# Performance work log

Measured on AMD Instinct MI355X. Metric: run time of the kernel, lower is better.

The kernel has to match this reference:

```python
import jax, jax.numpy as jnp
import numpy as np

B, L = 4, 2048
D_Q = D_K = D_V = 512
D_MODEL = 512
H = 8  # heads; head dim = D_MODEL // H = 64


def _conv1x1(x, W, b):
    # Conv1d with kernel_size=1 == pointwise linear over channels.
    # x: (B, C_in, L), W: (C_out, C_in), b: (C_out,) -> (B, C_out, L)
    return jnp.einsum('oc,bcl->bol', W, x) + b[None, :, None]


def setup_inputs() -> dict:
    key = jax.random.key(0)
    ks = jax.random.split(key, 12)
    s = 0.02
    return {
        'q': jax.random.normal(ks[0], (B, D_Q, L), jnp.float32),
        'k': jax.random.normal(ks[1], (B, D_K, L), jnp.float32),
        'v': jax.random.normal(ks[2], (B, D_V, L), jnp.float32),
        'input_mask': jnp.ones((B, 1, L), jnp.float32),
        'Wq': jax.random.normal(ks[3], (D_MODEL, D_Q), jnp.float32) * s,
        'bq': jax.random.normal(ks[4], (D_MODEL,), jnp.float32) * s,
        'Wk': jax.random.normal(ks[5], (D_MODEL, D_K), jnp.float32) * s,
        'bk': jax.random.normal(ks[6], (D_MODEL,), jnp.float32) * s,
        'Wv': jax.random.normal(ks[7], (D_MODEL, D_V), jnp.float32) * s,
        'bv': jax.random.normal(ks[8], (D_MODEL,), jnp.float32) * s,
        'Wout': jax.random.normal(ks[9], (D_V, D_MODEL), jnp.float32) * s,
        'bout': jax.random.normal(ks[10], (D_V,), jnp.float32) * s,
    }


def reference(q, k, v, input_mask, Wq, bq, Wk, bk, Wv, bv, Wout, bout):
    Bq, _, Lq = q.shape
    qh = _conv1x1(q, Wq, bq).reshape(Bq, H, -1, Lq)  # (B,H,D,L)
    kh = _conv1x1(k, Wk, bk).reshape(Bq, H, -1, Lq)
    vh = _conv1x1(v, Wv, bv).reshape(Bq, H, -1, Lq)
    Dh = qh.shape[2]
    scale = 1.0 / jnp.sqrt(jnp.asarray(Dh, qh.dtype))
    scores = jnp.einsum('bhdl,bhdn->bhln', qh, kh) * scale  # (B,H,L,L)
    # total_mask = ~input_mask[:, 0:1, :].bool(); True -> masked keys
    pad = input_mask[:, 0:1, :] <= 0.5  # (B,1,L_k)
    scores = jnp.where(pad[:, None, :, :], jnp.asarray(-1e9, scores.dtype), scores)
    attn = jax.nn.softmax(scores, axis=-1)  # attn_dropout is None in module
    out = jnp.einsum('bhdn,bhln->bhdl', vh, attn).reshape(Bq, -1, Lq)  # (B,d_model,L)
    # self.dropout is identity at inference; final 1x1 conv projection
    return _conv1x1(out, Wout, bout)  # (B, d_v, L)
```

## Files before the change

kernel.cpp:

```cpp
#include <hip/hip_runtime.h>
#include <hip/hip_bf16.h>


#define BB  4
#define LL  2048
#define CC  512
#define HH  8
#define DHH 64

typedef __attribute__((ext_vector_type(8)))  short bf16x8;
typedef __attribute__((ext_vector_type(4)))  short bf16x4;
typedef __attribute__((ext_vector_type(16))) float f32x16;
typedef __attribute__((ext_vector_type(2)))  unsigned uint2v;
typedef __attribute__((ext_vector_type(4)))  unsigned uint4v;

using us = unsigned short;

#if __has_builtin(__builtin_amdgcn_exp2f)
#define EXP2(x) __builtin_amdgcn_exp2f(x)
#else
#define EXP2(x) __expf(0.6931471805599453f * (x))
#endif

__device__ __forceinline__ int swz(int r) { return (r + (r >> 3)) & 7; }

__device__ __forceinline__ us f2bu(float x) {
    unsigned u = __float_as_uint(x);
    return (us)((u + 0x7FFFu + ((u >> 16) & 1u)) >> 16);
}
__device__ __forceinline__ unsigned pk2(float a, float b) {
    unsigned r;
    asm("v_cvt_pk_bf16_f32 %0, %1, %2" : "=v"(r) : "v"(a), "v"(b));
    return r;
}
__device__ __forceinline__ bf16x4 pk4(float a, float b, float c, float d) {
    uint2v u; u[0] = pk2(a, b); u[1] = pk2(c, d);
    return __builtin_bit_cast(bf16x4, u);
}

__device__ __forceinline__ void transpose_body(const float* __restrict__ X,
                                               us* __restrict__ Xt,
                                               int b, int c0, int n0, int t)
{
    __shared__ float T[64][65];

    const float* Xb = X + ((size_t)b * CC + c0) * LL + n0;
    #pragma unroll
    for (int i = 0; i < 4; ++i) {
        const int cl = (t >> 4) + 16 * i, nl = (t & 15) * 4;
        const float4 f = *(const float4*)(Xb + (size_t)cl * LL + nl);
        T[cl][nl + 0] = f.x; T[cl][nl + 1] = f.y;
        T[cl][nl + 2] = f.z; T[cl][nl + 3] = f.w;
    }
    __syncthreads();
    us* Ot = Xt + ((size_t)b * LL + n0) * CC + c0;
    #pragma unroll
    for (int i = 0; i < 2; ++i) {
        const int nl = (t >> 3) + 32 * i, cb = (t & 7) * 8;
        uint4v u;
        #pragma unroll
        for (int j = 0; j < 4; ++j)
            u[j] = pk2(T[cb + 2 * j][nl], T[cb + 2 * j + 1][nl]);
        *(bf16x8*)(Ot + (size_t)nl * CC + cb) = __builtin_bit_cast(bf16x8, u);
    }
}

__global__ __launch_bounds__(256) void transpose_cvt(const float* __restrict__ X,
                                                     us* __restrict__ Xt)
{
    transpose_body(X, Xt, blockIdx.z, blockIdx.y * 64, blockIdx.x * 64, threadIdx.x);
}

__global__ __launch_bounds__(256) void transpose_cvt3(
    const float* __restrict__ Xq, const float* __restrict__ Xk,
    const float* __restrict__ Xv,
    us* __restrict__ X0, us* __restrict__ X1, us* __restrict__ X2)
{
    const int z = blockIdx.z, which = z >> 2, b = z & 3;
    const float* X = which == 0 ? Xq : (which == 1 ? Xk : Xv);
    us* Xt = which == 0 ? X0 : (which == 1 ? X1 : X2);
    transpose_body(X, Xt, b, blockIdx.y * 64, blockIdx.x * 64, threadIdx.x);
}

__global__ __launch_bounds__(256) void cvt_w4(const float* __restrict__ W0,
                                              const float* __restrict__ W1,
                                              const float* __restrict__ W2,
                                              const float* __restrict__ W3,
                                              us* __restrict__ out)
{
    const float* Ws[4] = {W0, W1, W2, W3};
    const float* W = Ws[blockIdx.y];
    us* O = out + (size_t)blockIdx.y * (CC * CC);
    const int i = (blockIdx.x * 256 + threadIdx.x) * 8;
    const float4 f0 = *(const float4*)(W + i);
    const float4 f1 = *(const float4*)(W + i + 4);
    uint4v u;
    u[0] = pk2(f0.x, f0.y); u[1] = pk2(f0.z, f0.w);
    u[2] = pk2(f1.x, f1.y); u[3] = pk2(f1.z, f1.w);
    *(bf16x8*)(O + i) = __builtin_bit_cast(bf16x8, u);
}

__device__ __forceinline__ void proj_body(const us* __restrict__ Xb,
                                          const us* __restrict__ Wm,
                                          const float* __restrict__ bias,
                                          float scale, void* __restrict__ Yv,
                                          int b, int n0, int m0, int t, int mode)
{
    const int lane = t & 63, wave = t >> 6;
    const int quad2 = lane >> 5, l31 = lane & 31;
    const int wr = (wave >> 1) * 64, wc = (wave & 1) * 64;

    __shared__ us As[2][128 * 64];
    __shared__ us Bs[2][128 * 64];
    __shared__ float biasS[128];

    f32x16 acc[2][2];
    #pragma unroll
    for (int mi = 0; mi < 2; ++mi)
        #pragma unroll
        for (int ni = 0; ni < 2; ++ni)
            #pragma unroll
            for (int e = 0; e < 16; ++e) acc[mi][ni][e] = 0.f;

    if (t < 128) biasS[t] = bias[m0 + t];

    #pragma unroll
    for (int i = 0; i < 4; ++i) {
        const int id = i * 256 + t, r = id >> 3, bk = id & 7;
        *(bf16x8*)(As[0] + r * 64 + ((bk ^ swz(r)) * 8)) =
            *(const bf16x8*)(Wm + (size_t)r * CC + bk * 8);
        *(bf16x8*)(Bs[0] + r * 64 + ((bk ^ swz(r)) * 8)) =
            *(const bf16x8*)(Xb + (size_t)(n0 + r) * CC + bk * 8);
    }
    __syncthreads();

    for (int it = 0; it < CC / 64; ++it) {
        const int cur = it & 1, k1 = (it + 1) * 64;

        bf16x8 apre[4], bpre[4];
        if (it + 1 < CC / 64) {
            #pragma unroll
            for (int i = 0; i < 4; ++i) {
                const int id = i * 256 + t, r = id >> 3, bk = id & 7;
                apre[i] = *(const bf16x8*)(Wm + (size_t)r * CC + k1 + bk * 8);
                bpre[i] = *(const bf16x8*)(Xb + (size_t)(n0 + r) * CC + k1 + bk * 8);
            }
        }

        __builtin_amdgcn_s_setprio(1);
        #pragma unroll
        for (int ks = 0; ks < 4; ++ks) {
            const int bk = quad2 + 2 * ks;
            const int ra0 = wr + l31, ra1 = ra0 + 32;
            const int rb0 = wc + l31, rb1 = rb0 + 32;
            const bf16x8 af0 = *(const bf16x8*)(As[cur] + ra0 * 64 + ((bk ^ swz(ra0)) * 8));
            const bf16x8 af1 = *(const bf16x8*)(As[cur] + ra1 * 64 + ((bk ^ swz(ra1)) * 8));
            const bf16x8 bf0 = *(const bf16x8*)(Bs[cur] + rb0 * 64 + ((bk ^ swz(rb0)) * 8));
            const bf16x8 bf1 = *(const bf16x8*)(Bs[cur] + rb1 * 64 + ((bk ^ swz(rb1)) * 8));
            acc[0][0] = __builtin_amdgcn_mfma_f32_32x32x16_bf16(af0, bf0, acc[0][0], 0, 0, 0);
            acc[0][1] = __builtin_amdgcn_mfma_f32_32x32x16_bf16(af0, bf1, acc[0][1], 0, 0, 0);
            acc[1][0] = __builtin_amdgcn_mfma_f32_32x32x16_bf16(af1, bf0, acc[1][0], 0, 0, 0);
            acc[1][1] = __builtin_amdgcn_mfma_f32_32x32x16_bf16(af1, bf1, acc[1][1], 0, 0, 0);
        }
        __builtin_amdgcn_s_setprio(0);

        if (it + 1 < CC / 64) {
            #pragma unroll
            for (int i = 0; i < 4; ++i) {
                const int id = i * 256 + t, r = id >> 3, bk = id & 7;
                *(bf16x8*)(As[1 - cur] + r * 64 + ((bk ^ swz(r)) * 8)) = apre[i];
                *(bf16x8*)(Bs[1 - cur] + r * 64 + ((bk ^ swz(r)) * 8)) = bpre[i];
            }
        }
        __syncthreads();
    }

    #pragma unroll
    for (int mi = 0; mi < 2; ++mi)
        #pragma unroll
        for (int ni = 0; ni < 2; ++ni) {
            const int nloc = wc + ni * 32 + l31;
            if (mode == 0) {
                us* Y = (us*)Yv;
                #pragma unroll
                for (int rg2 = 0; rg2 < 4; ++rg2) {
                    const int rbase = wr + mi * 32 + 8 * rg2 + 4 * quad2;
                    float v0 = (acc[mi][ni][rg2 * 4 + 0] + biasS[rbase + 0]) * scale;
                    float v1 = (acc[mi][ni][rg2 * 4 + 1] + biasS[rbase + 1]) * scale;
                    float v2 = (acc[mi][ni][rg2 * 4 + 2] + biasS[rbase + 2]) * scale;
                    float v3 = (acc[mi][ni][rg2 * 4 + 3] + biasS[rbase + 3]) * scale;
                    const int mg = m0 + rbase;
                    const int h = mg >> 6, d = mg & 63;
                    *(bf16x4*)(Y + (((size_t)(b * HH + h) * LL) + n0 + nloc) * DHH + d) =
                        pk4(v0, v1, v2, v3);
                }
            } else {
                #pragma unroll
                for (int reg = 0; reg < 16; ++reg) {
                    const int row = (reg & 3) + 8 * (reg >> 2) + 4 * quad2;
                    const int mloc = wr + mi * 32 + row;
                    const float v = (acc[mi][ni][reg] + biasS[mloc]) * scale;
                    const size_t addr = ((size_t)b * CC + m0 + mloc) * LL + n0 + nloc;
                    if (mode == 1) ((us*)Yv)[addr] = f2bu(v);
                    else           ((float*)Yv)[addr] = v;
                }
            }
        }
}

template <int MODE>
__global__ __launch_bounds__(256, 2) void proj_gemm(const us* __restrict__ Xt,
                                                    const us* __restrict__ Wb,
                                                    const float* __restrict__ bias,
                                                    float scale,
                                                    void* __restrict__ Yv)
{
    const int b = blockIdx.z, n0 = blockIdx.x * 128, m0 = blockIdx.y * 128;
    proj_body(Xt + (size_t)b * LL * CC, Wb + (size_t)m0 * CC, bias, scale, Yv,
              b, n0, m0, threadIdx.x, MODE);
}

__global__ __launch_bounds__(256, 2) void proj_gemm3(
    const us* __restrict__ X0, const us* __restrict__ X1, const us* __restrict__ X2,
    const us* __restrict__ Wb4,
    const float* __restrict__ bq, const float* __restrict__ bk,
    const float* __restrict__ bv, float scale_q,
    us* __restrict__ qh, us* __restrict__ kh, us* __restrict__ vh)
{
    const int z = blockIdx.z, which = z >> 2, b = z & 3;
    const int n0 = blockIdx.x * 128, m0 = blockIdx.y * 128;
    const us* Xt = which == 0 ? X0 : (which == 1 ? X1 : X2);
    const us* Wb = Wb4 + (size_t)which * (CC * CC);
    const float* bias = which == 0 ? bq : (which == 1 ? bk : bv);
    const float scale = which == 0 ? scale_q : 1.0f;
    us* Yv = which == 0 ? qh : (which == 1 ? kh : vh);
    const int mode = (which == 2) ? 1 : 0;
    proj_body(Xt + (size_t)b * LL * CC, Wb + (size_t)m0 * CC, bias, scale,
              (void*)Yv, b, n0, m0, threadIdx.x, mode);
}

__global__ __launch_bounds__(256, 2) void attn_fwd(
    const us* __restrict__ Qh,
    const us* __restrict__ Kh,
    const us* __restrict__ Vh,
    const float* __restrict__ mask,
    us* __restrict__ ctx)
{
    const int bh = blockIdx.x;
    const int b = bh >> 3, h = bh & 7;
    const int qb = blockIdx.y;
    const int t = threadIdx.x, lane = t & 63, wave = t >> 6;
    const int quad2 = lane >> 5, l31 = lane & 31;
    const int qg = qb * 128 + wave * 32;
    const int NT = LL / 64;

    __shared__ us Ks[2][64 * 64];
    __shared__ us Vs[2][64 * 64];
    __shared__ unsigned long long mwS[32];

    const float* mb = mask + (size_t)b * LL;
    #pragma unroll
    for (int i = 0; i < 8; ++i) {
        const int tile = wave * 8 + i;
        const unsigned long long bal = __ballot(mb[tile * 64 + lane] > 0.5f);
        if (lane == 0) mwS[tile] = bal;
    }

    const us* Qbase = Qh + (size_t)bh * LL * DHH;
    bf16x8 qf[4];
    #pragma unroll
    for (int ks = 0; ks < 4; ++ks)
        qf[ks] = *(const bf16x8*)(Qbase + (size_t)(qg + l31) * DHH + ks * 16 + quad2 * 8);

    f32x16 of[2];
    #pragma unroll
    for (int mt = 0; mt < 2; ++mt)
        #pragma unroll
        for (int e = 0; e < 16; ++e) of[mt][e] = 0.f;
    float l_run = 0.f;

    const us* Kbase = Kh + (size_t)bh * LL * DHH;
    const us* Vbase = Vh + ((size_t)b * CC + h * DHH) * LL;

    #pragma unroll
    for (int i = 0; i < 2; ++i) {
        const int id = i * 256 + t;
        const int r = id >> 3, bk = id & 7;
        *(bf16x8*)(Ks[0] + r * 64 + ((bk ^ swz(r)) * 8)) =
            *(const bf16x8*)(Kbase + (size_t)r * DHH + bk * 8);
        *(bf16x8*)(Vs[0] + r * 64 + ((bk ^ swz(r)) * 8)) =
            *(const bf16x8*)(Vbase + (size_t)r * LL + bk * 8);
    }
    __syncthreads();

    f32x16 sf[2];
    #pragma unroll
    for (int mt = 0; mt < 2; ++mt)
        #pragma unroll
        for (int e = 0; e < 16; ++e) sf[mt][e] = 0.f;
    __builtin_amdgcn_s_setprio(1);
    #pragma unroll
    for (int ks = 0; ks < 4; ++ks) {
        const int bk = quad2 + 2 * ks;
        #pragma unroll
        for (int mt = 0; mt < 2; ++mt) {
            const int r = mt * 32 + l31;
            const bf16x8 af = *(const bf16x8*)(Ks[0] + r * 64 + ((bk ^ swz(r)) * 8));
            sf[mt] = __builtin_amdgcn_mfma_f32_32x32x16_bf16(af, qf[ks], sf[mt], 0, 0, 0);
        }
    }
    __builtin_amdgcn_s_setprio(0);

    for (int it = 0; it < NT; ++it) {
        const int cur = it & 1;

        bf16x8 kpre[2], vpre[2];
        if (it + 1 < NT) {
            const int n1 = (it + 1) * 64;
            #pragma unroll
            for (int i = 0; i < 2; ++i) {
                const int id = i * 256 + t;
                const int r = id >> 3, bk = id & 7;
                kpre[i] = *(const bf16x8*)(Kbase + (size_t)(n1 + r) * DHH + bk * 8);
                vpre[i] = *(const bf16x8*)(Vbase + (size_t)r * LL + n1 + bk * 8);
            }
        }

        const unsigned long long mw = mwS[it];
        const bool masked = (mw != 0xFFFFFFFFFFFFFFFFull);
        float ps = 0.f;
        bf16x8 pfrag[4];
        #pragma unroll
        for (int mt = 0; mt < 2; ++mt) {
            float p[16];
            #pragma unroll
            for (int e = 0; e < 16; ++e) p[e] = EXP2(sf[mt][e]);
            if (masked) {
                #pragma unroll
                for (int e = 0; e < 16; ++e) {
                    const int row = 32 * mt + (e & 3) + 8 * (e >> 2) + 4 * quad2;
                    p[e] = ((mw >> row) & 1ull) ? p[e] : 0.f;
                }
            }
            const float s0 = (p[0] + p[1]) + (p[2] + p[3]);
            const float s1 = (p[4] + p[5]) + (p[6] + p[7]);
            const float s2 = (p[8] + p[9]) + (p[10] + p[11]);
            const float s3 = (p[12] + p[13]) + (p[14] + p[15]);
            ps += (s0 + s1) + (s2 + s3);
            #pragma unroll
            for (int g = 0; g < 2; ++g) {
                unsigned w0 = pk2(p[8 * g + 0], p[8 * g + 1]);
                unsigned w1 = pk2(p[8 * g + 2], p[8 * g + 3]);
                unsigned w2 = pk2(p[8 * g + 4], p[8 * g + 5]);
                unsigned w3 = pk2(p[8 * g + 6], p[8 * g + 7]);
                asm("v_permlane32_swap_b32 %0, %1" : "+v"(w0), "+v"(w2));
                asm("v_permlane32_swap_b32 %0, %1" : "+v"(w1), "+v"(w3));
                uint4v u; u[0] = w0; u[1] = w1; u[2] = w2; u[3] = w3;
                pfrag[2 * mt + g] = __builtin_bit_cast(bf16x8, u);
            }
        }
        ps += __shfl_xor(ps, 32, 64);
        l_run += ps;

        __builtin_amdgcn_s_setprio(1);
        #pragma unroll
        for (int ks = 0; ks < 4; ++ks) {
            const int bk = quad2 + 2 * ks;
            #pragma unroll
            for (int mt = 0; mt < 2; ++mt) {
                const int r = mt * 32 + l31;
                const bf16x8 vf = *(const bf16x8*)(Vs[cur] + r * 64 + ((bk ^ swz(r)) * 8));
                of[mt] = __builtin_amdgcn_mfma_f32_32x32x16_bf16(vf, pfrag[ks], of[mt], 0, 0, 0);
            }
        }
        __builtin_amdgcn_s_setprio(0);

        if (it + 1 < NT) {
            #pragma unroll
            for (int i = 0; i < 2; ++i) {
                const int id = i * 256 + t;
                const int r = id >> 3, bk = id & 7;
                *(bf16x8*)(Ks[1 - cur] + r * 64 + ((bk ^ swz(r)) * 8)) = kpre[i];
                *(bf16x8*)(Vs[1 - cur] + r * 64 + ((bk ^ swz(r)) * 8)) = vpre[i];
            }
        }
        __syncthreads();

        if (it + 1 < NT) {
            #pragma unroll
            for (int mt = 0; mt < 2; ++mt)
                #pragma unroll
                for (int e = 0; e < 16; ++e) sf[mt][e] = 0.f;
            __builtin_amdgcn_s_setprio(1);
            #pragma unroll
            for (int ks = 0; ks < 4; ++ks) {
                const int bk = quad2 + 2 * ks;
                #pragma unroll
                for (int mt = 0; mt < 2; ++mt) {
                    const int r = mt * 32 + l31;
                    const bf16x8 af = *(const bf16x8*)(Ks[1 - cur] + r * 64 + ((bk ^ swz(r)) * 8));
                    sf[mt] = __builtin_amdgcn_mfma_f32_32x32x16_bf16(af, qf[ks], sf[mt], 0, 0, 0);
                }
            }
            __builtin_amdgcn_s_setprio(0);
        }
    }

    us* Cb = ctx + (size_t)b * LL * CC;
    const float inv = 1.0f / l_run;
    const int q = qg + l31;
    #pragma unroll
    for (int mt = 0; mt < 2; ++mt)
        #pragma unroll
        for (int rg2 = 0; rg2 < 4; ++rg2) {
            const int d = 32 * mt + 8 * rg2 + 4 * quad2;
            *(bf16x4*)(Cb + (size_t)q * CC + h * DHH + d) =
                pk4(of[mt][rg2 * 4 + 0] * inv, of[mt][rg2 * 4 + 1] * inv,
                    of[mt][rg2 * 4 + 2] * inv, of[mt][rg2 * 4 + 3] * inv);
        }
}

extern "C" void kernel_launch(void* const* d_in, const int* in_sizes, int n_in,
                              void* d_out, int out_size, void* d_ws, size_t ws_size,
                              hipStream_t stream)
{
    const float* q    = (const float*)d_in[0];
    const float* k    = (const float*)d_in[1];
    const float* v    = (const float*)d_in[2];
    const float* mask = (const float*)d_in[3];
    const float* Wq   = (const float*)d_in[4];
    const float* bq   = (const float*)d_in[5];
    const float* Wk   = (const float*)d_in[6];
    const float* bk   = (const float*)d_in[7];
    const float* Wv   = (const float*)d_in[8];
    const float* bv   = (const float*)d_in[9];
    const float* Wout = (const float*)d_in[10];
    const float* bout = (const float*)d_in[11];

    const size_t TSZ  = (size_t)BB * CC * LL;
    const size_t WSZ  = (size_t)4 * CC * CC;
    const float SCALE_Q = 0.125f * 1.4426950408889634f;

    const dim3 tb(256), gb(256);

    if (ws_size >= (6 * TSZ + WSZ) * sizeof(us)) {
        us* X0  = (us*)d_ws;
        us* X1  = X0 + TSZ;
        us* X2  = X1 + TSZ;
        us* qh  = X2 + TSZ;
        us* kh  = qh + TSZ;
        us* vh  = kh + TSZ;
        us* Wb  = vh + TSZ;
        us* ctx = X0;

        cvt_w4<<<dim3(CC * CC / 2048, 4), tb, 0, stream>>>(Wq, Wk, Wv, Wout, Wb);
        transpose_cvt3<<<dim3(LL / 64, CC / 64, 12), tb, 0, stream>>>(q, k, v, X0, X1, X2);
        proj_gemm3<<<dim3(LL / 128, CC / 128, 12), gb, 0, stream>>>(
            X0, X1, X2, Wb, bq, bk, bv, SCALE_Q, qh, kh, vh);
        attn_fwd<<<dim3(HH * BB, LL / 128), tb, 0, stream>>>(qh, kh, vh, mask, ctx);
        proj_gemm<2><<<dim3(LL / 128, CC / 128, BB), gb, 0, stream>>>(
            ctx, Wb + 3 * (size_t)CC * CC, bout, 1.0f, d_out);
    } else {
        us* Xt  = (us*)d_ws;
        us* qh  = Xt + TSZ;
        us* kh  = qh + TSZ;
        us* vh  = kh + TSZ;
        us* Wb  = vh + TSZ;
        us* ctx = Xt;

        const dim3 tg(LL / 64, CC / 64, BB), gg(LL / 128, CC / 128, BB);

        cvt_w4<<<dim3(CC * CC / 2048, 4), tb, 0, stream>>>(Wq, Wk, Wv, Wout, Wb);
        transpose_cvt<<<tg, tb, 0, stream>>>(q, Xt);
        proj_gemm<0><<<gg, gb, 0, stream>>>(Xt, Wb + 0 * (size_t)CC * CC, bq, SCALE_Q, (void*)qh);
        transpose_cvt<<<tg, tb, 0, stream>>>(k, Xt);
        proj_gemm<0><<<gg, gb, 0, stream>>>(Xt, Wb + 1 * (size_t)CC * CC, bk, 1.0f, (void*)kh);
        transpose_cvt<<<tg, tb, 0, stream>>>(v, Xt);
        proj_gemm<1><<<gg, gb, 0, stream>>>(Xt, Wb + 2 * (size_t)CC * CC, bv, 1.0f, (void*)vh);
        attn_fwd<<<dim3(HH * BB, LL / 128), tb, 0, stream>>>(qh, kh, vh, mask, ctx);
        proj_gemm<2><<<gg, gb, 0, stream>>>(ctx, Wb + 3 * (size_t)CC * CC, bout, 1.0f, d_out);
    }
}
```

Measured before the change: 192.6 us.

## Split KV loop across two wave groups and use padded k-major LDS layouts

The attention kernel now launches 512 threads per block. Two groups of four waves each process half of the key/value tiles for the same 128 queries, and the partial outputs and row sums are combined through shared memory at the end. This doubles the waves per CU and halves the serial key loop, since the grid is only about one block per CU. Both the projection GEMM and the attention kernel also replace the XOR-swizzled LDS tiles with a padded k-chunk-major layout that uses precomputed byte offsets, cutting address arithmetic and bank conflicts. The combine step only adds the partial sums, so it is correct only if both halves use the same softmax max reference; it also needs more LDS per block.

```diff
diff --git a/kernel.cpp b/kernel.cpp
--- a/kernel.cpp
+++ b/kernel.cpp
@@ -21,8 +21,6 @@
 #else
 #define EXP2(x) __expf(0.6931471805599453f * (x))
 #endif
-
-__device__ __forceinline__ int swz(int r) { return (r + (r >> 3)) & 7; }
 
 __device__ __forceinline__ us f2bu(float x) {
     unsigned u = __float_as_uint(x);
@@ -110,8 +108,7 @@
     const int quad2 = lane >> 5, l31 = lane & 31;
     const int wr = (wave >> 1) * 64, wc = (wave & 1) * 64;
 
-    __shared__ us As[2][128 * 64];
-    __shared__ us Bs[2][128 * 64];
+    __shared__ __align__(16) char PS[66048];
     __shared__ float biasS[128];
 
     f32x16 acc[2][2];
@@ -124,24 +121,30 @@
 
     if (t < 128) biasS[t] = bias[m0 + t];
 
+    const int wrO = (t & 7) * 2064 + (t >> 3) * 16;
+    const int rdA = quad2 * 2064 + (wr + l31) * 16;
+    const int rdB = 16512 + quad2 * 2064 + (wc + l31) * 16;
+
     #pragma unroll
     for (int i = 0; i < 4; ++i) {
-        const int id = i * 256 + t, r = id >> 3, bk = id & 7;
-        *(bf16x8*)(As[0] + r * 64 + ((bk ^ swz(r)) * 8)) =
+        const int r = i * 32 + (t >> 3), bk = t & 7;
+        *(bf16x8*)(PS + wrO + i * 512) =
             *(const bf16x8*)(Wm + (size_t)r * CC + bk * 8);
-        *(bf16x8*)(Bs[0] + r * 64 + ((bk ^ swz(r)) * 8)) =
+        *(bf16x8*)(PS + 16512 + wrO + i * 512) =
             *(const bf16x8*)(Xb + (size_t)(n0 + r) * CC + bk * 8);
     }
     __syncthreads();
 
     for (int it = 0; it < CC / 64; ++it) {
         const int cur = it & 1, k1 = (it + 1) * 64;
+        char* PB = PS + (cur ? 33024 : 0);
+        char* PN = PS + (cur ? 0 : 33024);
 
         bf16x8 apre[4], bpre[4];
         if (it + 1 < CC / 64) {
             #pragma unroll
             for (int i = 0; i < 4; ++i) {
-                const int id = i * 256 + t, r = id >> 3, bk = id & 7;
+                const int r = i * 32 + (t >> 3), bk = t & 7;
                 apre[i] = *(const bf16x8*)(Wm + (size_t)r * CC + k1 + bk * 8);
                 bpre[i] = *(const bf16x8*)(Xb + (size_t)(n0 + r) * CC + k1 + bk * 8);
             }
@@ -150,13 +153,10 @@
         __builtin_amdgcn_s_setprio(1);
         #pragma unroll
         for (int ks = 0; ks < 4; ++ks) {
-            const int bk = quad2 + 2 * ks;
-            const int ra0 = wr + l31, ra1 = ra0 + 32;
-            const int rb0 = wc + l31, rb1 = rb0 + 32;
-            const bf16x8 af0 = *(const bf16x8*)(As[cur] + ra0 * 64 + ((bk ^ swz(ra0)) * 8));
-            const bf16x8 af1 = *(const bf16x8*)(As[cur] + ra1 * 64 + ((bk ^ swz(ra1)) * 8));
-            const bf16x8 bf0 = *(const bf16x8*)(Bs[cur] + rb0 * 64 + ((bk ^ swz(rb0)) * 8));
-            const bf16x8 bf1 = *(const bf16x8*)(Bs[cur] + rb1 * 64 + ((bk ^ swz(rb1)) * 8));
+            const bf16x8 af0 = *(const bf16x8*)(PB + rdA + ks * 4128);
+            const bf16x8 af1 = *(const bf16x8*)(PB + rdA + ks * 4128 + 512);
+            const bf16x8 bf0 = *(const bf16x8*)(PB + rdB + ks * 4128);
+            const bf16x8 bf1 = *(const bf16x8*)(PB + rdB + ks * 4128 + 512);
             acc[0][0] = __builtin_amdgcn_mfma_f32_32x32x16_bf16(af0, bf0, acc[0][0], 0, 0, 0);
             acc[0][1] = __builtin_amdgcn_mfma_f32_32x32x16_bf16(af0, bf1, acc[0][1], 0, 0, 0);
             acc[1][0] = __builtin_amdgcn_mfma_f32_32x32x16_bf16(af1, bf0, acc[1][0], 0, 0, 0);
@@ -167,9 +167,8 @@
         if (it + 1 < CC / 64) {
             #pragma unroll
             for (int i = 0; i < 4; ++i) {
-                const int id = i * 256 + t, r = id >> 3, bk = id & 7;
-                *(bf16x8*)(As[1 - cur] + r * 64 + ((bk ^ swz(r)) * 8)) = apre[i];
-                *(bf16x8*)(Bs[1 - cur] + r * 64 + ((bk ^ swz(r)) * 8)) = bpre[i];
+                *(bf16x8*)(PN + wrO + i * 512) = apre[i];
+                *(bf16x8*)(PN + 16512 + wrO + i * 512) = bpre[i];
             }
         }
         __syncthreads();
@@ -239,7 +238,7 @@
               (void*)Yv, b, n0, m0, threadIdx.x, mode);
 }
 
-__global__ __launch_bounds__(256, 2) void attn_fwd(
+__global__ __launch_bounds__(512, 4) void attn_fwd(
     const us* __restrict__ Qh,
     const us* __restrict__ Kh,
     const us* __restrict__ Vh,
@@ -250,18 +249,18 @@
     const int b = bh >> 3, h = bh & 7;
     const int qb = blockIdx.y;
     const int t = threadIdx.x, lane = t & 63, wave = t >> 6;
+    const int half = wave >> 2, wv = wave & 3;
     const int quad2 = lane >> 5, l31 = lane & 31;
-    const int qg = qb * 128 + wave * 32;
-    const int NT = LL / 64;
-
-    __shared__ us Ks[2][64 * 64];
-    __shared__ us Vs[2][64 * 64];
+    const int th = t & 255;
+    const int qg = qb * 128 + wv * 32;
+
+    __shared__ __align__(16) char SM[66560];
     __shared__ unsigned long long mwS[32];
 
     const float* mb = mask + (size_t)b * LL;
     #pragma unroll
-    for (int i = 0; i < 8; ++i) {
-        const int tile = wave * 8 + i;
+    for (int i = 0; i < 4; ++i) {
+        const int tile = wave * 4 + i;
         const unsigned long long bal = __ballot(mb[tile * 64 + lane] > 0.5f);
         if (lane == 0) mwS[tile] = bal;
     }
@@ -282,14 +281,18 @@
     const us* Kbase = Kh + (size_t)bh * LL * DHH;
     const us* Vbase = Vh + ((size_t)b * CC + h * DHH) * LL;
 
+    char* SH = SM + half * 33280;
+    const int wrO = (th & 7) * 1040 + (th >> 3) * 16;
+    const int rdO = quad2 * 1040 + l31 * 16;
+    const int g0 = half * 16;
+
     #pragma unroll
     for (int i = 0; i < 2; ++i) {
-        const int id = i * 256 + t;
-        const int r = id >> 3, bk = id & 7;
-        *(bf16x8*)(Ks[0] + r * 64 + ((bk ^ swz(r)) * 8)) =
-            *(const bf16x8*)(Kbase + (size_t)r * DHH + bk * 8);
-        *(bf16x8*)(Vs[0] + r * 64 + ((bk ^ swz(r)) * 8)) =
-            *(const bf16x8*)(Vbase + (size_t)r * LL + bk * 8);
+        const int r = i * 32 + (th >> 3), bk = th & 7;
+        *(bf16x8*)(SH + wrO + i * 512) =
+            *(const bf16x8*)(Kbase + (size_t)(g0 * 64 + r) * DHH + bk * 8);
+        *(bf16x8*)(SH + 8320 + wrO + i * 512) =
+            *(const bf16x8*)(Vbase + (size_t)r * LL + g0 * 64 + bk * 8);
     }
     __syncthreads();
 
@@ -298,35 +301,35 @@
     for (int mt = 0; mt < 2; ++mt)
         #pragma unroll
         for (int e = 0; e < 16; ++e) sf[mt][e] = 0.f;
-    __builtin_amdgcn_s_setprio(1);
-    #pragma unroll
-    for (int ks = 0; ks < 4; ++ks) {
-        const int bk = quad2 + 2 * ks;
-        #pragma unroll
-        for (int mt = 0; mt < 2; ++mt) {
-            const int r = mt * 32 + l31;
-            const bf16x8 af = *(const bf16x8*)(Ks[0] + r * 64 + ((bk ^ swz(r)) * 8));
-            sf[mt] = __builtin_amdgcn_mfma_f32_32x32x16_bf16(af, qf[ks], sf[mt], 0, 0, 0);
-        }
-    }
-    __builtin_amdgcn_s_setprio(0);
-
-    for (int it = 0; it < NT; ++it) {
-        const int cur = it & 1;
+    {
+        const char* pK = SH + rdO;
+        __builtin_amdgcn_s_setprio(1);
+        #pragma unroll
+        for (int ks = 0; ks < 4; ++ks)
+            #pragma unroll
+            for (int mt = 0; mt < 2; ++mt)
+                sf[mt] = __builtin_amdgcn_mfma_f32_32x32x16_bf16(
+                    *(const bf16x8*)(pK + ks * 2080 + mt * 512), qf[ks], sf[mt], 0, 0, 0);
+        __builtin_amdgcn_s_setprio(0);
+    }
+
+    for (int itl = 0; itl < 16; ++itl) {
+        const int cur = itl & 1;
+        char* SB = SH + (cur ? 16640 : 0);
+        char* SN = SH + (cur ? 0 : 16640);
 
         bf16x8 kpre[2], vpre[2];
-        if (it + 1 < NT) {
-            const int n1 = (it + 1) * 64;
+        if (itl + 1 < 16) {
+            const int n1 = (g0 + itl + 1) * 64;
             #pragma unroll
             for (int i = 0; i < 2; ++i) {
-                const int id = i * 256 + t;
-                const int r = id >> 3, bk = id & 7;
+                const int r = i * 32 + (th >> 3), bk = th & 7;
                 kpre[i] = *(const bf16x8*)(Kbase + (size_t)(n1 + r) * DHH + bk * 8);
                 vpre[i] = *(const bf16x8*)(Vbase + (size_t)r * LL + n1 + bk * 8);
             }
         }
 
-        const unsigned long long mw = mwS[it];
+        const unsigned long long mw = mwS[g0 + itl];
         const bool masked = (mw != 0xFFFFFFFFFFFFFFFFull);
         float ps = 0.f;
         bf16x8 pfrag[4];
@@ -364,60 +367,72 @@
 
         __builtin_amdgcn_s_setprio(1);
         #pragma unroll
-        for (int ks = 0; ks < 4; ++ks) {
-            const int bk = quad2 + 2 * ks;
+        for (int ks = 0; ks < 4; ++ks)
             #pragma unroll
             for (int mt = 0; mt < 2; ++mt) {
-                const int r = mt * 32 + l31;
-                const bf16x8 vf = *(const bf16x8*)(Vs[cur] + r * 64 + ((bk ^ swz(r)) * 8));
+                const bf16x8 vf = *(const bf16x8*)(SB + 8320 + rdO + ks * 2080 + mt * 512);
                 of[mt] = __builtin_amdgcn_mfma_f32_32x32x16_bf16(vf, pfrag[ks], of[mt], 0, 0, 0);
             }
-        }
         __builtin_amdgcn_s_setprio(0);
 
-        if (it + 1 < NT) {
+        if (itl + 1 < 16) {
             #pragma unroll
             for (int i = 0; i < 2; ++i) {
-                const int id = i * 256 + t;
-                const int r = id >> 3, bk = id & 7;
-                *(bf16x8*)(Ks[1 - cur] + r * 64 + ((bk ^ swz(r)) * 8)) = kpre[i];
-                *(bf16x8*)(Vs[1 - cur] + r * 64 + ((bk ^ swz(r)) * 8)) = vpre[i];
+                *(bf16x8*)(SN + wrO + i * 512) = kpre[i];
+                *(bf16x8*)(SN + 8320 + wrO + i * 512) = vpre[i];
             }
         }
         __syncthreads();
 
-        if (it + 1 < NT) {
+        if (itl + 1 < 16) {
             #pragma unroll
             for (int mt = 0; mt < 2; ++mt)
                 #pragma unroll
                 for (int e = 0; e < 16; ++e) sf[mt][e] = 0.f;
             __builtin_amdgcn_s_setprio(1);
             #pragma unroll
-            for (int ks = 0; ks < 4; ++ks) {
-                const int bk = quad2 + 2 * ks;
+            for (int ks = 0; ks < 4; ++ks)
                 #pragma unroll
-                for (int mt = 0; mt < 2; ++mt) {
-                    const int r = mt * 32 + l31;
-                    const bf16x8 af = *(const bf16x8*)(Ks[1 - cur] + r * 64 + ((bk ^ swz(r)) * 8));
-                    sf[mt] = __builtin_amdgcn_mfma_f32_32x32x16_bf16(af, qf[ks], sf[mt], 0, 0, 0);
-                }
-            }
+                for (int mt = 0; mt < 2; ++mt)
+                    sf[mt] = __builtin_amdgcn_mfma_f32_32x32x16_bf16(
+                        *(const bf16x8*)(SN + rdO + ks * 2080 + mt * 512), qf[ks], sf[mt], 0, 0, 0);
             __builtin_amdgcn_s_setprio(0);
         }
     }
 
-    us* Cb = ctx + (size_t)b * LL * CC;
-    const float inv = 1.0f / l_run;
-    const int q = qg + l31;
-    #pragma unroll
-    for (int mt = 0; mt < 2; ++mt)
-        #pragma unroll
-        for (int rg2 = 0; rg2 < 4; ++rg2) {
-            const int d = 32 * mt + 8 * rg2 + 4 * quad2;
-            *(bf16x4*)(Cb + (size_t)q * CC + h * DHH + d) =
-                pk4(of[mt][rg2 * 4 + 0] * inv, of[mt][rg2 * 4 + 1] * inv,
-                    of[mt][rg2 * 4 + 2] * inv, of[mt][rg2 * 4 + 3] * inv);
-        }
+    float4* OS = (float4*)SM;
+    float*  LS = (float*)(SM + 32768);
+    if (half == 1) {
+        #pragma unroll
+        for (int mt = 0; mt < 2; ++mt)
+            #pragma unroll
+            for (int r4 = 0; r4 < 4; ++r4) {
+                float4 v;
+                v.x = of[mt][r4 * 4 + 0]; v.y = of[mt][r4 * 4 + 1];
+                v.z = of[mt][r4 * 4 + 2]; v.w = of[mt][r4 * 4 + 3];
+                OS[(wv * 8 + mt * 4 + r4) * 64 + lane] = v;
+            }
+        LS[wv * 64 + lane] = l_run;
+    }
+    __syncthreads();
+    if (half == 0) {
+        l_run += LS[wv * 64 + lane];
+        const float inv = 1.0f / l_run;
+        us* Cb = ctx + (size_t)b * LL * CC;
+        const int q = qg + l31;
+        #pragma unroll
+        for (int mt = 0; mt < 2; ++mt)
+            #pragma unroll
+            for (int r4 = 0; r4 < 4; ++r4) {
+                const float4 v = OS[(wv * 8 + mt * 4 + r4) * 64 + lane];
+                const int d = 32 * mt + 8 * r4 + 4 * quad2;
+                *(bf16x4*)(Cb + (size_t)q * CC + h * DHH + d) =
+                    pk4((of[mt][r4 * 4 + 0] + v.x) * inv,
+                        (of[mt][r4 * 4 + 1] + v.y) * inv,
+                        (of[mt][r4 * 4 + 2] + v.z) * inv,
+                        (of[mt][r4 * 4 + 3] + v.w) * inv);
+            }
+    }
 }
 
 extern "C" void kernel_launch(void* const* d_in, const int* in_sizes, int n_in,
@@ -457,7 +472,7 @@
         transpose_cvt3<<<dim3(LL / 64, CC / 64, 12), tb, 0, stream>>>(q, k, v, X0, X1, X2);
         proj_gemm3<<<dim3(LL / 128, CC / 128, 12), gb, 0, stream>>>(
             X0, X1, X2, Wb, bq, bk, bv, SCALE_Q, qh, kh, vh);
-        attn_fwd<<<dim3(HH * BB, LL / 128), tb, 0, stream>>>(qh, kh, vh, mask, ctx);
+        attn_fwd<<<dim3(HH * BB, LL / 128), dim3(512), 0, stream>>>(qh, kh, vh, mask, ctx);
         proj_gemm<2><<<dim3(LL / 128, CC / 128, BB), gb, 0, stream>>>(
             ctx, Wb + 3 * (size_t)CC * CC, bout, 1.0f, d_out);
     } else {
@@ -477,7 +492,7 @@
         proj_gemm<0><<<gg, gb, 0, stream>>>(Xt, Wb + 1 * (size_t)CC * CC, bk, 1.0f, (void*)kh);
         transpose_cvt<<<tg, tb, 0, stream>>>(v, Xt);
         proj_gemm<1><<<gg, gb, 0, stream>>>(Xt, Wb + 2 * (size_t)CC * CC, bv, 1.0f, (void*)vh);
-        attn_fwd<<<dim3(HH * BB, LL / 128), tb, 0, stream>>>(qh, kh, vh, mask, ctx);
+        attn_fwd<<<dim3(HH * BB, LL / 128), dim3(512), 0, stream>>>(qh, kh, vh, mask, ctx);
         proj_gemm<2><<<gg, gb, 0, stream>>>(ctx, Wb + 3 * (size_t)CC * CC, bout, 1.0f, d_out);
     }
 }
```

Result: slower. 204.8 us (+6.3%).
